# Performance work log

Measured on AMD Instinct MI355X. Metric: run time of the kernel, lower is better.

Reference implementation:

```python
import jax, jax.numpy as jnp
import numpy as np

N_HEAD = 4
EPS = 1e-5

def _layernorm(x, g, b):
    mu = jnp.mean(x, axis=-1, keepdims=True)
    var = jnp.mean(jnp.square(x - mu), axis=-1, keepdims=True)
    return (x - mu) * jax.lax.rsqrt(var + EPS) * g + b

def setup_inputs() -> dict:
    key = jax.random.key(0)
    ks = jax.random.split(key, 16)
    B, T, F = 8, 1024, 256
    dk = F // N_HEAD
    s = 1.0 / np.sqrt(F)
    return {
        "x": jax.random.normal(ks[0], (B, T, F), jnp.float32),
        "q_in": jax.random.normal(ks[1], (B, T, F), jnp.float32),
        "pos_k": jax.random.normal(ks[2], (T, T, dk), jnp.float32),
        "mask": jax.random.randint(ks[3], (B, T, T), 0, 2, jnp.int32),
        "ln_g": jnp.ones((F,), jnp.float32),
        "ln_b": jnp.zeros((F,), jnp.float32),
        "Wq": jax.random.normal(ks[4], (F, F), jnp.float32) * s,
        "bq": jnp.zeros((F,), jnp.float32),
        "Wk": jax.random.normal(ks[5], (F, F), jnp.float32) * s,
        "bk": jnp.zeros((F,), jnp.float32),
        "Wv": jax.random.normal(ks[6], (F, F), jnp.float32) * s,
        "bv": jnp.zeros((F,), jnp.float32),
        "Wo": jax.random.normal(ks[7], (F, F), jnp.float32) * s,
        "bo": jnp.zeros((F,), jnp.float32),
    }

def reference(x, q_in, pos_k, mask, ln_g, ln_b, Wq, bq, Wk, bk, Wv, bv, Wo, bo):
    B, T2, F = x.shape
    T1 = q_in.shape[1]
    h = N_HEAD
    dk = F // h
    xn = _layernorm(x, ln_g, ln_b)
    # (B, T, h, dk) -> (B, h, T, dk)
    q = (q_in @ Wq + bq).reshape(B, T1, h, dk).transpose(0, 2, 1, 3)
    k = (xn @ Wk + bk).reshape(B, T2, h, dk).transpose(0, 2, 1, 3)
    v = (xn @ Wv + bv).reshape(B, T2, h, dk).transpose(0, 2, 1, 3)
    A = jnp.einsum('bhqd,bhkd->bhqk', q, k)
    # relative position bias: B[b,h,q,t] = sum_d q[b,h,q,d] * pos_k[q,t,d]
    Bmat = jnp.einsum('bhqd,qtd->bhqt', q, pos_k)
    scores = (A + Bmat) / np.sqrt(dk)
    m = (mask[:, None, :, :] == 0)  # (B,1,T1,T2)
    min_val = jnp.finfo(scores.dtype).min
    scores = jnp.where(m, min_val, scores)
    attn = jax.nn.softmax(scores, axis=-1)
    attn = jnp.where(m, 0.0, attn)
    out = jnp.einsum('bhqk,bhkd->bhqd', attn, v)
    out = out.transpose(0, 2, 1, 3).reshape(B, T1, F)
    return out @ Wo + bo
```

## Files before the change

kernel.cpp:

```cpp
#include <hip/hip_runtime.h>
#include <hip/hip_bf16.h>

#define TT 1024
#define FF 256

typedef float  f4v  __attribute__((ext_vector_type(4)));
typedef float  f16v __attribute__((ext_vector_type(16)));
typedef __bf16 bf8v __attribute__((ext_vector_type(8)));
typedef unsigned short us8v __attribute__((ext_vector_type(8)));
typedef unsigned short us4v __attribute__((ext_vector_type(4)));

static __device__ __forceinline__ unsigned short f2bf(float x) {
    return __builtin_bit_cast(unsigned short, (__bf16)x);
}
static __device__ __forceinline__ float bf2f(unsigned short u) {
    return (float)__builtin_bit_cast(__bf16, u);
}
static __device__ __forceinline__ bf8v us2bf(us8v v) {
    return __builtin_bit_cast(bf8v, v);
}

__global__ __launch_bounds__(256) void k_wprep(
    const float* __restrict__ Wq, const float* __restrict__ Wk,
    const float* __restrict__ Wv, const float* __restrict__ Wo,
    unsigned short* __restrict__ Wt)
{
    __shared__ unsigned short T[32][36];
    const float* W = (blockIdx.y == 0) ? Wq : (blockIdx.y == 1) ? Wk
                   : (blockIdx.y == 2) ? Wv : Wo;
    unsigned short* dst = Wt + (blockIdx.y << 16);
    const int kt = (blockIdx.x >> 3) << 5, nt = (blockIdx.x & 7) << 5;
    const int r = threadIdx.x >> 3, c0 = (threadIdx.x & 7) << 2;
    const f4v w = *(const f4v*)&W[(kt + r) * FF + nt + c0];
    #pragma unroll
    for (int j = 0; j < 4; ++j) T[c0 + j][r] = f2bf(w[j]);
    __syncthreads();
    *(us4v*)&dst[(nt + r) * FF + kt + c0] = *(const us4v*)&T[r][c0];
}

__global__ __launch_bounds__(256) void k_ln(
    const float* __restrict__ x, const float* __restrict__ qin,
    const float* __restrict__ lng, const float* __restrict__ lnb,
    unsigned short* __restrict__ xn_bf, unsigned short* __restrict__ qin_bf)
{
    const int tid = threadIdx.x, lane = tid & 63, wv = tid >> 6;
    const int r0 = blockIdx.x << 4;

    #pragma unroll
    for (int u = 0; u < 4; ++u) {
        const int i4 = ((u << 8) + tid) << 2;
        const int r = i4 >> 8, c = i4 & 255;
        const f4v qv = *(const f4v*)&qin[(r0 + r) * FF + c];
        us4v o;
        #pragma unroll
        for (int j = 0; j < 4; ++j) o[j] = f2bf(qv[j]);
        *(us4v*)&qin_bf[(r0 + r) * FF + c] = o;
    }

    #pragma unroll
    for (int rr = 0; rr < 4; ++rr) {
        const int row = r0 + (wv << 2) + rr;
        float v[4], s = 0.f, s2 = 0.f;
        #pragma unroll
        for (int c4 = 0; c4 < 4; ++c4) {
            v[c4] = x[row * FF + (c4 << 6) + lane];
            s += v[c4]; s2 += v[c4] * v[c4];
        }
        #pragma unroll
        for (int off = 1; off < 64; off <<= 1) {
            s  += __shfl_xor(s, off);
            s2 += __shfl_xor(s2, off);
        }
        const float mu  = s * (1.f / FF);
        const float rsd = rsqrtf(s2 * (1.f / FF) - mu * mu + 1e-5f);
        #pragma unroll
        for (int c4 = 0; c4 < 4; ++c4) {
            const int c = (c4 << 6) + lane;
            xn_bf[row * FF + c] = f2bf((v[c4] - mu) * rsd * lng[c] + lnb[c]);
        }
    }
}

__global__ __launch_bounds__(256) void k_proj(
    const unsigned short* __restrict__ qin_bf, const unsigned short* __restrict__ xn_bf,
    const unsigned short* __restrict__ Wt,
    const float* __restrict__ bq, const float* __restrict__ bk, const float* __restrict__ bv,
    unsigned short* __restrict__ Qh, unsigned short* __restrict__ Kh,
    unsigned short* __restrict__ Vt)
{
    __shared__ __align__(16) unsigned short As[64 * 264];
    const int z = blockIdx.y;
    const unsigned short* A = (z == 0) ? qin_bf : xn_bf;
    const unsigned short* W = Wt + (z << 16);
    const float* bias = (z == 0) ? bq : (z == 1) ? bk : bv;
    unsigned short* dst = (z == 0) ? Qh : (z == 1) ? Kh : Vt;
    const int tid = threadIdx.x;
    const int m0 = blockIdx.x << 6;

    #pragma unroll
    for (int u = 0; u < 8; ++u) {
        const int idx = (u << 8) + tid;
        const int r = idx >> 5, c = (idx & 31) << 3;
        *(us8v*)&As[r * 264 + c] = *(const us8v*)&A[(m0 + r) * FF + c];
    }
    __syncthreads();

    const int lane = tid & 63, nw = tid >> 6, gq = lane >> 5, l31 = lane & 31;
    f16v acc[2][2];
    #pragma unroll
    for (int i = 0; i < 2; ++i)
        #pragma unroll
        for (int j = 0; j < 2; ++j)
            #pragma unroll
            for (int e = 0; e < 16; ++e) acc[i][j][e] = 0.f;

    for (int ks = 0; ks < 16; ++ks) {
        const int k0 = (ks << 4) + (gq << 3);
        bf8v af[2], wf[2];
        af[0] = us2bf(*(const us8v*)&As[l31 * 264 + k0]);
        af[1] = us2bf(*(const us8v*)&As[(32 + l31) * 264 + k0]);
        wf[0] = us2bf(*(const us8v*)&W[((nw << 6) + l31) * FF + k0]);
        wf[1] = us2bf(*(const us8v*)&W[((nw << 6) + 32 + l31) * FF + k0]);
        if (z == 2) {
            #pragma unroll
            for (int ti = 0; ti < 2; ++ti)
                #pragma unroll
                for (int tj = 0; tj < 2; ++tj)
                    acc[ti][tj] = __builtin_amdgcn_mfma_f32_32x32x16_bf16(
                        wf[tj], af[ti], acc[ti][tj], 0, 0, 0);
        } else {
            #pragma unroll
            for (int ti = 0; ti < 2; ++ti)
                #pragma unroll
                for (int tj = 0; tj < 2; ++tj)
                    acc[ti][tj] = __builtin_amdgcn_mfma_f32_32x32x16_bf16(
                        af[ti], wf[tj], acc[ti][tj], 0, 0, 0);
        }
    }

    if (z != 2) {
        #pragma unroll
        for (int ti = 0; ti < 2; ++ti)
            #pragma unroll
            for (int tj = 0; tj < 2; ++tj)
                #pragma unroll
                for (int reg = 0; reg < 16; ++reg) {
                    const int row = (reg & 3) + ((reg >> 2) << 3) + (gq << 2);
                    const int tg = m0 + (ti << 5) + row;
                    const int n = (nw << 6) + (tj << 5) + l31;
                    float val = acc[ti][tj][reg] + bias[n];
                    if (z == 0) val *= 0.125f;
                    const int b = tg >> 10, t = tg & 1023;
                    dst[(((b << 2) + nw) << 16) + (t << 6) + (tj << 5) + l31] = f2bf(val);
                }
    } else {
        #pragma unroll
        for (int ti = 0; ti < 2; ++ti)
            #pragma unroll
            for (int tj = 0; tj < 2; ++tj)
                #pragma unroll
                for (int reg = 0; reg < 16; ++reg) {
                    const int row = (reg & 3) + ((reg >> 2) << 3) + (gq << 2);
                    const int d = (tj << 5) + row;
                    const int tg = m0 + (ti << 5) + l31;
                    const float val = acc[ti][tj][reg] + bias[(nw << 6) + d];
                    const int b = tg >> 10, t = tg & 1023;
                    dst[(((b << 2) + nw) << 16) + (d << 10) + t] = f2bf(val);
                }
    }
}

__global__ __launch_bounds__(256) void k_bterm(
    const unsigned short* __restrict__ Qh, const float* __restrict__ posk,
    const int* __restrict__ mask, unsigned short* __restrict__ Bm)
{
    const int tid = threadIdx.x, lane = tid & 63, wv = tid >> 6;
    const int gq = lane >> 5, m = lane & 31;
    const int q = blockIdx.y;
    const int t = (blockIdx.x << 7) + (wv << 5) + m;

    bf8v afr[4];
    #pragma unroll
    for (int kk = 0; kk < 4; ++kk)
        afr[kk] = us2bf(*(const us8v*)&Qh[(m << 16) + (q << 6) + (kk << 4) + (gq << 3)]);

    bf8v bfr[4];
    #pragma unroll
    for (int kk = 0; kk < 4; ++kk) {
        const int d0 = (kk << 4) + (gq << 3);
        const f4v p0 = *(const f4v*)&posk[(((q << 10) + t) << 6) + d0];
        const f4v p1 = *(const f4v*)&posk[(((q << 10) + t) << 6) + d0 + 4];
        bf8v bb;
        bb[0] = (__bf16)p0[0]; bb[1] = (__bf16)p0[1];
        bb[2] = (__bf16)p0[2]; bb[3] = (__bf16)p0[3];
        bb[4] = (__bf16)p1[0]; bb[5] = (__bf16)p1[1];
        bb[6] = (__bf16)p1[2]; bb[7] = (__bf16)p1[3];
        bfr[kk] = bb;
    }

    f16v acc;
    #pragma unroll
    for (int i = 0; i < 16; ++i) acc[i] = 0.f;
    #pragma unroll
    for (int kk = 0; kk < 4; ++kk)
        acc = __builtin_amdgcn_mfma_f32_32x32x16_bf16(afr[kk], bfr[kk], acc, 0, 0, 0);

    int mk[4];
    #pragma unroll
    for (int g = 0; g < 4; ++g)
        mk[g] = mask[(((g << 1) + gq) << 20) + (q << 10) + t];
    #pragma unroll
    for (int reg = 0; reg < 16; ++reg) {
        const int g = reg >> 2;
        const int bhr = (reg & 3) + (g << 3) + (gq << 2);
        const float val = mk[g] ? acc[reg] : -3.0e38f;
        Bm[(bhr << 20) + (q << 10) + t] = f2bf(val);
    }
}

__global__ __launch_bounds__(256, 4) void k_attn(
    const unsigned short* __restrict__ Qh, const unsigned short* __restrict__ Kh,
    const unsigned short* __restrict__ Vt, const unsigned short* __restrict__ Bm,
    unsigned short* __restrict__ aout_bf)
{
    __shared__ __align__(16) unsigned short Qs[32 * 72];
    __shared__ __align__(16) unsigned short Ps[32 * 136];
    __shared__ __align__(16) unsigned short Bs[2][32 * 136];
    __shared__ float wmax[4][32], wsum[4][32];

    const int tid = threadIdx.x, lane = tid & 63, wv = tid >> 6;
    const int l15 = lane & 15, quad = lane >> 4;
    const int blk = blockIdx.x;
    const int bh = ((blk & 7) << 2) | ((blk >> 3) & 3);
    const int qt = blk >> 5;
    const int b = bh >> 2, h = bh & 3;
    const int q0 = qt << 5;

    {
        const int r = tid >> 3, d0 = (tid & 7) << 3;
        *(us8v*)&Qs[r * 72 + d0] =
            *(const us8v*)&Qh[(bh << 16) + ((q0 + r) << 6) + d0];
    }
    {
        #pragma unroll
        for (int u = 0; u < 2; ++u) {
            const int idx = (u << 8) + tid;
            const int r = idx >> 4, c = (idx & 15) << 3;
            *(us8v*)&Bs[0][r * 136 + c] =
                *(const us8v*)&Bm[(bh << 20) + ((q0 + r) << 10) + c];
        }
    }
    __syncthreads();

    f4v o0, o1;
    float mreg[2][4], lreg[2][4], alpha[2][4];
    #pragma unroll
    for (int i = 0; i < 4; ++i) { o0[i] = 0.f; o1[i] = 0.f; }
    #pragma unroll
    for (int mf = 0; mf < 2; ++mf)
        #pragma unroll
        for (int r = 0; r < 4; ++r) { mreg[mf][r] = -3.0e38f; lreg[mf][r] = 0.f; }

    for (int it = 0; it < 8; ++it) {
        const int t0 = it << 7;
        const int cur = it & 1;

        us8v pf[2];
        if (it < 7) {
            #pragma unroll
            for (int u = 0; u < 2; ++u) {
                const int idx = (u << 8) + tid;
                const int r = idx >> 4, c = (idx & 15) << 3;
                pf[u] = *(const us8v*)&Bm[(bh << 20) + ((q0 + r) << 10) + t0 + 128 + c];
            }
        }

        if (it > 0) {
            #pragma unroll
            for (int mf = 0; mf < 2; ++mf)
                #pragma unroll
                for (int r = 0; r < 4; ++r) {
                    const int q = (mf << 4) + (quad << 2) + r;
                    lreg[mf][r] += (wsum[0][q] + wsum[1][q]) + (wsum[2][q] + wsum[3][q]);
                }
        }

        f4v s00, s01, s10, s11;
        #pragma unroll
        for (int i = 0; i < 4; ++i) { s00[i]=0.f; s01[i]=0.f; s10[i]=0.f; s11[i]=0.f; }
        #pragma unroll
        for (int kk = 0; kk < 2; ++kk) {
            const int d0 = (kk << 5) + (quad << 3);
            const bf8v aq0 = us2bf(*(const us8v*)&Qs[l15 * 72 + d0]);
            const bf8v aq1 = us2bf(*(const us8v*)&Qs[(16 + l15) * 72 + d0]);
            const bf8v kb0 = us2bf(*(const us8v*)&Kh[(bh << 16) + ((t0 + (wv << 5) + l15) << 6) + d0]);
            const bf8v kb1 = us2bf(*(const us8v*)&Kh[(bh << 16) + ((t0 + (wv << 5) + 16 + l15) << 6) + d0]);
            s00 = __builtin_amdgcn_mfma_f32_16x16x32_bf16(aq0, kb0, s00, 0, 0, 0);
            s01 = __builtin_amdgcn_mfma_f32_16x16x32_bf16(aq0, kb1, s01, 0, 0, 0);
            s10 = __builtin_amdgcn_mfma_f32_16x16x32_bf16(aq1, kb0, s10, 0, 0, 0);
            s11 = __builtin_amdgcn_mfma_f32_16x16x32_bf16(aq1, kb1, s11, 0, 0, 0);
        }

        float sv[2][2][4];
        #pragma unroll
        for (int mf = 0; mf < 2; ++mf)
            #pragma unroll
            for (int nf = 0; nf < 2; ++nf) {
                const f4v sfr = (mf == 0) ? (nf == 0 ? s00 : s01)
                                          : (nf == 0 ? s10 : s11);
                const int tl = (wv << 5) + (nf << 4) + l15;
                #pragma unroll
                for (int r = 0; r < 4; ++r) {
                    const int q = (mf << 4) + (quad << 2) + r;
                    sv[mf][nf][r] = sfr[r] + bf2f(Bs[cur][q * 136 + tl]);
                }
            }

        #pragma unroll
        for (int mf = 0; mf < 2; ++mf)
            #pragma unroll
            for (int r = 0; r < 4; ++r) {
                float vx = fmaxf(sv[mf][0][r], sv[mf][1][r]);
                vx = fmaxf(vx, __shfl_xor(vx, 1));
                vx = fmaxf(vx, __shfl_xor(vx, 2));
                vx = fmaxf(vx, __shfl_xor(vx, 4));
                vx = fmaxf(vx, __shfl_xor(vx, 8));
                if (l15 == 0) wmax[wv][(mf << 4) + (quad << 2) + r] = vx;
            }
        if (it < 7) {
            #pragma unroll
            for (int u = 0; u < 2; ++u) {
                const int idx = (u << 8) + tid;
                const int r = idx >> 4, c = (idx & 15) << 3;
                *(us8v*)&Bs[cur ^ 1][r * 136 + c] = pf[u];
            }
        }
        __syncthreads();

        #pragma unroll
        for (int mf = 0; mf < 2; ++mf)
            #pragma unroll
            for (int r = 0; r < 4; ++r) {
                const int q = (mf << 4) + (quad << 2) + r;
                const float tm = fmaxf(fmaxf(wmax[0][q], wmax[1][q]),
                                       fmaxf(wmax[2][q], wmax[3][q]));
                const float mo = mreg[mf][r];
                const float mn = fmaxf(mo, tm);
                alpha[mf][r] = __expf(mo - mn);
                mreg[mf][r] = mn;
            }
        #pragma unroll
        for (int mf = 0; mf < 2; ++mf)
            #pragma unroll
            for (int r = 0; r < 4; ++r) {
                const int q = (mf << 4) + (quad << 2) + r;
                const float p0 = __expf(sv[mf][0][r] - mreg[mf][r]);
                const float p1 = __expf(sv[mf][1][r] - mreg[mf][r]);
                Ps[q * 136 + (wv << 5) + l15]      = f2bf(p0);
                Ps[q * 136 + (wv << 5) + 16 + l15] = f2bf(p1);
                float rs2 = p0 + p1;
                rs2 += __shfl_xor(rs2, 1);
                rs2 += __shfl_xor(rs2, 2);
                rs2 += __shfl_xor(rs2, 4);
                rs2 += __shfl_xor(rs2, 8);
                if (l15 == 0) wsum[wv][q] = rs2;
            }
        #pragma unroll
        for (int r = 0; r < 4; ++r) { o0[r] *= alpha[0][r]; o1[r] *= alpha[1][r]; }
        #pragma unroll
        for (int mf = 0; mf < 2; ++mf)
            #pragma unroll
            for (int r = 0; r < 4; ++r) lreg[mf][r] *= alpha[mf][r];
        __syncthreads();

        #pragma unroll
        for (int kk = 0; kk < 4; ++kk) {
            const int toff = (kk << 5) + (quad << 3);
            const bf8v vbf = us2bf(*(const us8v*)&Vt[(bh << 16) + (((wv << 4) + l15) << 10) + t0 + toff]);
            const bf8v ap0 = us2bf(*(const us8v*)&Ps[l15 * 136 + toff]);
            const bf8v ap1 = us2bf(*(const us8v*)&Ps[(16 + l15) * 136 + toff]);
            o0 = __builtin_amdgcn_mfma_f32_16x16x32_bf16(ap0, vbf, o0, 0, 0, 0);
            o1 = __builtin_amdgcn_mfma_f32_16x16x32_bf16(ap1, vbf, o1, 0, 0, 0);
        }
    }

    #pragma unroll
    for (int mf = 0; mf < 2; ++mf)
        #pragma unroll
        for (int r = 0; r < 4; ++r) {
            const int q = (mf << 4) + (quad << 2) + r;
            lreg[mf][r] += (wsum[0][q] + wsum[1][q]) + (wsum[2][q] + wsum[3][q]);
        }

    const int d = (wv << 4) + l15;
    #pragma unroll
    for (int mf = 0; mf < 2; ++mf)
        #pragma unroll
        for (int r = 0; r < 4; ++r) {
            const int q = (mf << 4) + (quad << 2) + r;
            const float ov = ((mf == 0) ? o0[r] : o1[r]) / lreg[mf][r];
            aout_bf[((b << 10) + q0 + q) * FF + (h << 6) + d] = f2bf(ov);
        }
}

__global__ __launch_bounds__(256) void k_oproj(
    const unsigned short* __restrict__ aout_bf, const unsigned short* __restrict__ Wot,
    const float* __restrict__ bo, float* __restrict__ out)
{
    __shared__ __align__(16) unsigned short As[64 * 264];
    const int tid = threadIdx.x;
    const int m0 = blockIdx.x << 6;

    #pragma unroll
    for (int u = 0; u < 8; ++u) {
        const int idx = (u << 8) + tid;
        const int r = idx >> 5, c = (idx & 31) << 3;
        *(us8v*)&As[r * 264 + c] = *(const us8v*)&aout_bf[(m0 + r) * FF + c];
    }
    __syncthreads();

    const int lane = tid & 63, nw = tid >> 6, gq = lane >> 5, l31 = lane & 31;
    f16v acc[2][2];
    #pragma unroll
    for (int i = 0; i < 2; ++i)
        #pragma unroll
        for (int j = 0; j < 2; ++j)
            #pragma unroll
            for (int e = 0; e < 16; ++e) acc[i][j][e] = 0.f;

    for (int ks = 0; ks < 16; ++ks) {
        const int k0 = (ks << 4) + (gq << 3);
        bf8v af[2], wf[2];
        af[0] = us2bf(*(const us8v*)&As[l31 * 264 + k0]);
        af[1] = us2bf(*(const us8v*)&As[(32 + l31) * 264 + k0]);
        wf[0] = us2bf(*(const us8v*)&Wot[((nw << 6) + l31) * FF + k0]);
        wf[1] = us2bf(*(const us8v*)&Wot[((nw << 6) + 32 + l31) * FF + k0]);
        #pragma unroll
        for (int ti = 0; ti < 2; ++ti)
            #pragma unroll
            for (int tj = 0; tj < 2; ++tj)
                acc[ti][tj] = __builtin_amdgcn_mfma_f32_32x32x16_bf16(
                    af[ti], wf[tj], acc[ti][tj], 0, 0, 0);
    }

    #pragma unroll
    for (int ti = 0; ti < 2; ++ti)
        #pragma unroll
        for (int tj = 0; tj < 2; ++tj)
            #pragma unroll
            for (int reg = 0; reg < 16; ++reg) {
                const int row = (reg & 3) + ((reg >> 2) << 3) + (gq << 2);
                const int tg = m0 + (ti << 5) + row;
                const int n = (nw << 6) + (tj << 5) + l31;
                out[tg * FF + n] = acc[ti][tj][reg] + bo[n];
            }
}

extern "C" void kernel_launch(void* const* d_in, const int* in_sizes, int n_in,
                              void* d_out, int out_size, void* d_ws, size_t ws_size,
                              hipStream_t stream)
{
    const float* x    = (const float*)d_in[0];
    const float* qin  = (const float*)d_in[1];
    const float* posk = (const float*)d_in[2];
    const int*   mask = (const int*)d_in[3];
    const float* ln_g = (const float*)d_in[4];
    const float* ln_b = (const float*)d_in[5];
    const float* Wq   = (const float*)d_in[6];
    const float* bq   = (const float*)d_in[7];
    const float* Wk   = (const float*)d_in[8];
    const float* bk   = (const float*)d_in[9];
    const float* Wv   = (const float*)d_in[10];
    const float* bv   = (const float*)d_in[11];
    const float* Wo   = (const float*)d_in[12];
    const float* bo   = (const float*)d_in[13];
    float* out = (float*)d_out;

    char* ws = (char*)d_ws;
    unsigned short* wWt   = (unsigned short*)(ws);
    unsigned short* qinb  = (unsigned short*)(ws + (size_t)(1u << 20));
    unsigned short* xnb   = (unsigned short*)(ws + (size_t)(5u << 20));
    unsigned short* Qh    = (unsigned short*)(ws + (size_t)(9u << 20));
    unsigned short* Kh    = (unsigned short*)(ws + (size_t)(13u << 20));
    unsigned short* Vth   = (unsigned short*)(ws + (size_t)(17u << 20));
    unsigned short* aoutb = (unsigned short*)(ws + (size_t)(21u << 20));
    unsigned short* Bm    = (unsigned short*)(ws + (size_t)(25u << 20));

    hipLaunchKernelGGL(k_wprep, dim3(64, 4), dim3(256), 0, stream, Wq, Wk, Wv, Wo, wWt);
    hipLaunchKernelGGL(k_ln, dim3(512), dim3(256), 0, stream,
                       x, qin, ln_g, ln_b, xnb, qinb);
    hipLaunchKernelGGL(k_proj, dim3(128, 3), dim3(256), 0, stream,
                       qinb, xnb, wWt, bq, bk, bv, Qh, Kh, Vth);
    hipLaunchKernelGGL(k_bterm, dim3(8, 1024), dim3(256), 0, stream,
                       Qh, posk, mask, Bm);
    hipLaunchKernelGGL(k_attn, dim3(1024), dim3(256), 0, stream,
                       Qh, Kh, Vth, Bm, aoutb);
    hipLaunchKernelGGL(k_oproj, dim3(128), dim3(256), 0, stream,
                       aoutb, wWt + (3 << 16), bo, out);
}
```

Baseline: 533.3 us.

## Restructure attention kernel to per-wave split-KV flash attention without block barriers

Rewrites the attention kernel so each wave owns 16 query rows and half of the key range, keeping Q fragments in registers and computing S^T via MFMA with K as the A operand. Softmax max and sum reductions now stay within a wave, which removes the per-iteration LDS exchanges and two __syncthreads per tile. The bias tile is read straight from global memory instead of being staged through shared memory, and P goes through a small per-wave LDS buffer. The two key halves are merged once at the end through LDS. The cost is more registers (8 score fragments plus 4 output accumulators), which may reduce occupancy, and bias loads are no longer prefetched.

```diff
diff --git a/kernel.cpp b/kernel.cpp
--- a/kernel.cpp
+++ b/kernel.cpp
@@ -223,184 +223,135 @@
     const unsigned short* __restrict__ Vt, const unsigned short* __restrict__ Bm,
     unsigned short* __restrict__ aout_bf)
 {
-    __shared__ __align__(16) unsigned short Qs[32 * 72];
-    __shared__ __align__(16) unsigned short Ps[32 * 136];
-    __shared__ __align__(16) unsigned short Bs[2][32 * 136];
-    __shared__ float wmax[4][32], wsum[4][32];
+    __shared__ __align__(16) unsigned short PsT[4][16 * 132];
+    __shared__ __align__(16) float OLDS[2][16 * 68];
+    __shared__ float MLDS[2][2][16];
 
     const int tid = threadIdx.x, lane = tid & 63, wv = tid >> 6;
     const int l15 = lane & 15, quad = lane >> 4;
+    const int qg = wv & 1, th = wv >> 1;
     const int blk = blockIdx.x;
     const int bh = ((blk & 7) << 2) | ((blk >> 3) & 3);
     const int qt = blk >> 5;
     const int b = bh >> 2, h = bh & 3;
-    const int q0 = qt << 5;
-
+    const int q0w = (qt << 5) + (qg << 4);
+
+    bf8v qb0, qb1;
     {
-        const int r = tid >> 3, d0 = (tid & 7) << 3;
-        *(us8v*)&Qs[r * 72 + d0] =
-            *(const us8v*)&Qh[(bh << 16) + ((q0 + r) << 6) + d0];
-    }
-    {
-        #pragma unroll
-        for (int u = 0; u < 2; ++u) {
-            const int idx = (u << 8) + tid;
-            const int r = idx >> 4, c = (idx & 15) << 3;
-            *(us8v*)&Bs[0][r * 136 + c] =
-                *(const us8v*)&Bm[(bh << 20) + ((q0 + r) << 10) + c];
-        }
+        const int base = (bh << 16) + ((q0w + l15) << 6) + (quad << 3);
+        qb0 = us2bf(*(const us8v*)&Qh[base]);
+        qb1 = us2bf(*(const us8v*)&Qh[base + 32]);
+    }
+
+    f4v O[4];
+    #pragma unroll
+    for (int i = 0; i < 4; ++i) { O[i][0]=0.f; O[i][1]=0.f; O[i][2]=0.f; O[i][3]=0.f; }
+    float m_run = -3.0e38f, l_run = 0.f;
+
+    for (int cc = 0; cc < 4; ++cc) {
+        const int t0c = (th << 9) + (cc << 7);
+
+        f4v s[8];
+        #pragma unroll
+        for (int nf = 0; nf < 8; ++nf) {
+            const int krow = (bh << 16) + ((t0c + (nf << 4) + l15) << 6) + (quad << 3);
+            const bf8v ka0 = us2bf(*(const us8v*)&Kh[krow]);
+            const bf8v ka1 = us2bf(*(const us8v*)&Kh[krow + 32]);
+            f4v z;
+            z[0]=0.f; z[1]=0.f; z[2]=0.f; z[3]=0.f;
+            z = __builtin_amdgcn_mfma_f32_16x16x32_bf16(ka0, qb0, z, 0, 0, 0);
+            z = __builtin_amdgcn_mfma_f32_16x16x32_bf16(ka1, qb1, z, 0, 0, 0);
+            s[nf] = z;
+        }
+
+        #pragma unroll
+        for (int nf = 0; nf < 8; ++nf) {
+            const us4v bm = *(const us4v*)&Bm[(bh << 20) + ((q0w + l15) << 10)
+                                             + t0c + (nf << 4) + (quad << 2)];
+            #pragma unroll
+            for (int r = 0; r < 4; ++r) s[nf][r] += bf2f(bm[r]);
+        }
+
+        f4v mx = s[0];
+        #pragma unroll
+        for (int nf = 1; nf < 8; ++nf) {
+            mx[0] = fmaxf(mx[0], s[nf][0]); mx[1] = fmaxf(mx[1], s[nf][1]);
+            mx[2] = fmaxf(mx[2], s[nf][2]); mx[3] = fmaxf(mx[3], s[nf][3]);
+        }
+        float cm = fmaxf(fmaxf(mx[0], mx[1]), fmaxf(mx[2], mx[3]));
+        cm = fmaxf(cm, __shfl_xor(cm, 16));
+        cm = fmaxf(cm, __shfl_xor(cm, 32));
+
+        const float mn = fmaxf(m_run, cm);
+        const float alpha = __expf(m_run - mn);
+        m_run = mn;
+        l_run *= alpha;
+        #pragma unroll
+        for (int i = 0; i < 4; ++i) {
+            O[i][0] *= alpha; O[i][1] *= alpha; O[i][2] *= alpha; O[i][3] *= alpha;
+        }
+
+        float rs = 0.f;
+        #pragma unroll
+        for (int nf = 0; nf < 8; ++nf) {
+            const float p0 = __expf(s[nf][0] - mn);
+            const float p1 = __expf(s[nf][1] - mn);
+            const float p2 = __expf(s[nf][2] - mn);
+            const float p3 = __expf(s[nf][3] - mn);
+            const int ea = l15 * 132 + (nf << 4) + (quad << 2);
+            *(unsigned int*)&PsT[wv][ea] =
+                (unsigned int)f2bf(p0) | ((unsigned int)f2bf(p1) << 16);
+            *(unsigned int*)&PsT[wv][ea + 2] =
+                (unsigned int)f2bf(p2) | ((unsigned int)f2bf(p3) << 16);
+            rs += (p0 + p1) + (p2 + p3);
+        }
+        rs += __shfl_xor(rs, 16);
+        rs += __shfl_xor(rs, 32);
+        l_run += rs;
+
+        #pragma unroll
+        for (int tc = 0; tc < 4; ++tc) {
+            const int eb = l15 * 132 + (tc << 5) + (quad << 3);
+            const us4v plo = *(const us4v*)&PsT[wv][eb];
+            const us4v phi = *(const us4v*)&PsT[wv][eb + 4];
+            us8v pc;
+            pc[0]=plo[0]; pc[1]=plo[1]; pc[2]=plo[2]; pc[3]=plo[3];
+            pc[4]=phi[0]; pc[5]=phi[1]; pc[6]=phi[2]; pc[7]=phi[3];
+            const bf8v pb = us2bf(pc);
+            #pragma unroll
+            for (int dt = 0; dt < 4; ++dt) {
+                const bf8v va = us2bf(*(const us8v*)&Vt[(bh << 16)
+                    + (((dt << 4) + l15) << 10) + t0c + (tc << 5) + (quad << 3)]);
+                O[dt] = __builtin_amdgcn_mfma_f32_16x16x32_bf16(va, pb, O[dt], 0, 0, 0);
+            }
+        }
+    }
+
+    if (th == 1) {
+        #pragma unroll
+        for (int dt = 0; dt < 4; ++dt)
+            *(f4v*)&OLDS[qg][l15 * 68 + (dt << 4) + (quad << 2)] = O[dt];
+        if (quad == 0) { MLDS[qg][0][l15] = m_run; MLDS[qg][1][l15] = l_run; }
     }
     __syncthreads();
-
-    f4v o0, o1;
-    float mreg[2][4], lreg[2][4], alpha[2][4];
-    #pragma unroll
-    for (int i = 0; i < 4; ++i) { o0[i] = 0.f; o1[i] = 0.f; }
-    #pragma unroll
-    for (int mf = 0; mf < 2; ++mf)
-        #pragma unroll
-        for (int r = 0; r < 4; ++r) { mreg[mf][r] = -3.0e38f; lreg[mf][r] = 0.f; }
-
-    for (int it = 0; it < 8; ++it) {
-        const int t0 = it << 7;
-        const int cur = it & 1;
-
-        us8v pf[2];
-        if (it < 7) {
-            #pragma unroll
-            for (int u = 0; u < 2; ++u) {
-                const int idx = (u << 8) + tid;
-                const int r = idx >> 4, c = (idx & 15) << 3;
-                pf[u] = *(const us8v*)&Bm[(bh << 20) + ((q0 + r) << 10) + t0 + 128 + c];
-            }
-        }
-
-        if (it > 0) {
-            #pragma unroll
-            for (int mf = 0; mf < 2; ++mf)
-                #pragma unroll
-                for (int r = 0; r < 4; ++r) {
-                    const int q = (mf << 4) + (quad << 2) + r;
-                    lreg[mf][r] += (wsum[0][q] + wsum[1][q]) + (wsum[2][q] + wsum[3][q]);
-                }
-        }
-
-        f4v s00, s01, s10, s11;
-        #pragma unroll
-        for (int i = 0; i < 4; ++i) { s00[i]=0.f; s01[i]=0.f; s10[i]=0.f; s11[i]=0.f; }
-        #pragma unroll
-        for (int kk = 0; kk < 2; ++kk) {
-            const int d0 = (kk << 5) + (quad << 3);
-            const bf8v aq0 = us2bf(*(const us8v*)&Qs[l15 * 72 + d0]);
-            const bf8v aq1 = us2bf(*(const us8v*)&Qs[(16 + l15) * 72 + d0]);
-            const bf8v kb0 = us2bf(*(const us8v*)&Kh[(bh << 16) + ((t0 + (wv << 5) + l15) << 6) + d0]);
-            const bf8v kb1 = us2bf(*(const us8v*)&Kh[(bh << 16) + ((t0 + (wv << 5) + 16 + l15) << 6) + d0]);
-            s00 = __builtin_amdgcn_mfma_f32_16x16x32_bf16(aq0, kb0, s00, 0, 0, 0);
-            s01 = __builtin_amdgcn_mfma_f32_16x16x32_bf16(aq0, kb1, s01, 0, 0, 0);
-            s10 = __builtin_amdgcn_mfma_f32_16x16x32_bf16(aq1, kb0, s10, 0, 0, 0);
-            s11 = __builtin_amdgcn_mfma_f32_16x16x32_bf16(aq1, kb1, s11, 0, 0, 0);
-        }
-
-        float sv[2][2][4];
-        #pragma unroll
-        for (int mf = 0; mf < 2; ++mf)
-            #pragma unroll
-            for (int nf = 0; nf < 2; ++nf) {
-                const f4v sfr = (mf == 0) ? (nf == 0 ? s00 : s01)
-                                          : (nf == 0 ? s10 : s11);
-                const int tl = (wv << 5) + (nf << 4) + l15;
-                #pragma unroll
-                for (int r = 0; r < 4; ++r) {
-                    const int q = (mf << 4) + (quad << 2) + r;
-                    sv[mf][nf][r] = sfr[r] + bf2f(Bs[cur][q * 136 + tl]);
-                }
-            }
-
-        #pragma unroll
-        for (int mf = 0; mf < 2; ++mf)
-            #pragma unroll
-            for (int r = 0; r < 4; ++r) {
-                float vx = fmaxf(sv[mf][0][r], sv[mf][1][r]);
-                vx = fmaxf(vx, __shfl_xor(vx, 1));
-                vx = fmaxf(vx, __shfl_xor(vx, 2));
-                vx = fmaxf(vx, __shfl_xor(vx, 4));
-                vx = fmaxf(vx, __shfl_xor(vx, 8));
-                if (l15 == 0) wmax[wv][(mf << 4) + (quad << 2) + r] = vx;
-            }
-        if (it < 7) {
-            #pragma unroll
-            for (int u = 0; u < 2; ++u) {
-                const int idx = (u << 8) + tid;
-                const int r = idx >> 4, c = (idx & 15) << 3;
-                *(us8v*)&Bs[cur ^ 1][r * 136 + c] = pf[u];
-            }
-        }
-        __syncthreads();
-
-        #pragma unroll
-        for (int mf = 0; mf < 2; ++mf)
-            #pragma unroll
-            for (int r = 0; r < 4; ++r) {
-                const int q = (mf << 4) + (quad << 2) + r;
-                const float tm = fmaxf(fmaxf(wmax[0][q], wmax[1][q]),
-                                       fmaxf(wmax[2][q], wmax[3][q]));
-                const float mo = mreg[mf][r];
-                const float mn = fmaxf(mo, tm);
-                alpha[mf][r] = __expf(mo - mn);
-                mreg[mf][r] = mn;
-            }
-        #pragma unroll
-        for (int mf = 0; mf < 2; ++mf)
-            #pragma unroll
-            for (int r = 0; r < 4; ++r) {
-                const int q = (mf << 4) + (quad << 2) + r;
-                const float p0 = __expf(sv[mf][0][r] - mreg[mf][r]);
-                const float p1 = __expf(sv[mf][1][r] - mreg[mf][r]);
-                Ps[q * 136 + (wv << 5) + l15]      = f2bf(p0);
-                Ps[q * 136 + (wv << 5) + 16 + l15] = f2bf(p1);
-                float rs2 = p0 + p1;
-                rs2 += __shfl_xor(rs2, 1);
-                rs2 += __shfl_xor(rs2, 2);
-                rs2 += __shfl_xor(rs2, 4);
-                rs2 += __shfl_xor(rs2, 8);
-                if (l15 == 0) wsum[wv][q] = rs2;
-            }
-        #pragma unroll
-        for (int r = 0; r < 4; ++r) { o0[r] *= alpha[0][r]; o1[r] *= alpha[1][r]; }
-        #pragma unroll
-        for (int mf = 0; mf < 2; ++mf)
-            #pragma unroll
-            for (int r = 0; r < 4; ++r) lreg[mf][r] *= alpha[mf][r];
-        __syncthreads();
-
-        #pragma unroll
-        for (int kk = 0; kk < 4; ++kk) {
-            const int toff = (kk << 5) + (quad << 3);
-            const bf8v vbf = us2bf(*(const us8v*)&Vt[(bh << 16) + (((wv << 4) + l15) << 10) + t0 + toff]);
-            const bf8v ap0 = us2bf(*(const us8v*)&Ps[l15 * 136 + toff]);
-            const bf8v ap1 = us2bf(*(const us8v*)&Ps[(16 + l15) * 136 + toff]);
-            o0 = __builtin_amdgcn_mfma_f32_16x16x32_bf16(ap0, vbf, o0, 0, 0, 0);
-            o1 = __builtin_amdgcn_mfma_f32_16x16x32_bf16(ap1, vbf, o1, 0, 0, 0);
-        }
-    }
-
-    #pragma unroll
-    for (int mf = 0; mf < 2; ++mf)
-        #pragma unroll
-        for (int r = 0; r < 4; ++r) {
-            const int q = (mf << 4) + (quad << 2) + r;
-            lreg[mf][r] += (wsum[0][q] + wsum[1][q]) + (wsum[2][q] + wsum[3][q]);
-        }
-
-    const int d = (wv << 4) + l15;
-    #pragma unroll
-    for (int mf = 0; mf < 2; ++mf)
-        #pragma unroll
-        for (int r = 0; r < 4; ++r) {
-            const int q = (mf << 4) + (quad << 2) + r;
-            const float ov = ((mf == 0) ? o0[r] : o1[r]) / lreg[mf][r];
-            aout_bf[((b << 10) + q0 + q) * FF + (h << 6) + d] = f2bf(ov);
-        }
+    if (th == 0) {
+        const float m1 = MLDS[qg][0][l15];
+        const float l1 = MLDS[qg][1][l15];
+        const float mm = fmaxf(m_run, m1);
+        const float a0 = __expf(m_run - mm);
+        const float a1 = __expf(m1 - mm);
+        const float linv = 1.f / (l_run * a0 + l1 * a1);
+        const int orow = ((b << 10) + q0w + l15) * FF + (h << 6);
+        #pragma unroll
+        for (int dt = 0; dt < 4; ++dt) {
+            const f4v o1 = *(const f4v*)&OLDS[qg][l15 * 68 + (dt << 4) + (quad << 2)];
+            us4v ov;
+            #pragma unroll
+            for (int r = 0; r < 4; ++r)
+                ov[r] = f2bf((O[dt][r] * a0 + o1[r] * a1) * linv);
+            *(us4v*)&aout_bf[orow + (dt << 4) + (quad << 2)] = ov;
+        }
+    }
 }
 
 __global__ __launch_bounds__(256) void k_oproj(
```

New measurement: 530.3 us. Within noise of the previous version (-0.5%).
